# Kernel tuning notes

Measured on AMD Instinct MI355X. Metric: run time of the kernel, lower is better.

The kernel has to match this reference:

```python
import jax, jax.numpy as jnp
import numpy as np

N_NODES = 50000

def sage_conv(x, src, dst, W_l, b_l, W_r):
    # mean-aggregate neighbor features x[src] at dst, then lin_l(agg)+lin_r(x)
    msgs = x[src]                                       # [E, d]
    agg = jax.ops.segment_sum(msgs, dst, num_segments=N_NODES)
    cnt = jax.ops.segment_sum(jnp.ones((src.shape[0],), x.dtype), dst, num_segments=N_NODES)
    agg = agg / jnp.maximum(cnt, 1.0)[:, None]          # [N, d]
    return agg @ W_l.T + b_l + x @ W_r.T


def setup_inputs() -> dict:
    key = jax.random.key(0)
    ks = jax.random.split(key, 10)
    in_c, hid, out_c = 128, 128, 64
    x = jax.random.normal(ks[0], (N_NODES, in_c), dtype=jnp.float32)
    edge_index = jax.random.randint(ks[1], (2, 800000), 0, N_NODES, dtype=jnp.int64)
    s = 1.0 / np.sqrt(in_c)
    W1_l = jax.random.uniform(ks[2], (hid, in_c), minval=-s, maxval=s)
    b1 = jax.random.uniform(ks[3], (hid,), minval=-s, maxval=s)
    W1_r = jax.random.uniform(ks[4], (hid, in_c), minval=-s, maxval=s)
    s = 1.0 / np.sqrt(hid)
    W2_l = jax.random.uniform(ks[5], (hid, hid), minval=-s, maxval=s)
    b2 = jax.random.uniform(ks[6], (hid,), minval=-s, maxval=s)
    W2_r = jax.random.uniform(ks[7], (hid, hid), minval=-s, maxval=s)
    W3 = jax.random.uniform(ks[8], (out_c, hid), minval=-s, maxval=s)
    b3 = jax.random.uniform(ks[9], (out_c,), minval=-s, maxval=s)
    return {"x": x, "edge_index": edge_index, "W1_l": W1_l, "b1": b1, "W1_r": W1_r,
            "W2_l": W2_l, "b2": b2, "W2_r": W2_r, "W3": W3, "b3": b3}


def reference(x, edge_index, W1_l, b1, W1_r, W2_l, b2, W2_r, W3, b3):
    src, dst = edge_index[0], edge_index[1]
    h = jax.nn.relu(sage_conv(x, src, dst, W1_l, b1, W1_r))
    h = jax.nn.relu(sage_conv(h, src, dst, W2_l, b2, W2_r))
    return h @ W3.T + b3
```

## Files before the change

### kernel.cpp

```cpp
#include <hip/hip_runtime.h>

#define FDIM 128

typedef __attribute__((ext_vector_type(8))) short bf16x8;
typedef __attribute__((ext_vector_type(4))) float f32x4;

static __device__ __forceinline__ ushort f2bf(float f) {
    uint u = __float_as_uint(f);
    uint r = (u + 0x7FFF + ((u >> 16) & 1)) >> 16;
    return (ushort)r;
}
static __device__ __forceinline__ uint packbf(float lo, float hi) {
    return (uint)f2bf(lo) | ((uint)f2bf(hi) << 16);
}
static __device__ __forceinline__ float bflo(uint v) { return __uint_as_float(v << 16); }
static __device__ __forceinline__ float bfhi(uint v) { return __uint_as_float(v & 0xFFFF0000u); }


__global__ void prep_kernel(const float* __restrict__ x, ushort* __restrict__ xb, int nx8,
                            const float* __restrict__ W1l, const float* __restrict__ W1r,
                            const float* __restrict__ W2l, const float* __restrict__ W2r,
                            const float* __restrict__ W3, ushort* __restrict__ wbuf,
                            const int* __restrict__ dst, int E, int* __restrict__ bcnt,
                            int nconv) {
    const int b = blockIdx.x;
    const int tid = threadIdx.x;
    if (b < nconv) {
        int i = b * 256 + tid;
        if (i < nx8) {
            const float* s = x + (size_t)i * 8;
            float4 a = *(const float4*)(s);
            float4 c = *(const float4*)(s + 4);
            uint4 o;
            o.x = packbf(a.x, a.y); o.y = packbf(a.z, a.w);
            o.z = packbf(c.x, c.y); o.w = packbf(c.z, c.w);
            *(uint4*)(xb + (size_t)i * 8) = o;
        }
    } else if (b < nconv + 36) {
        int c = (b - nconv) * 256 + tid;
        const float* s; ushort* d;
        if (c < 2048)      { s = W1l + (size_t)c * 8;          d = wbuf + (size_t)c * 8; }
        else if (c < 4096) { s = W1r + (size_t)(c - 2048) * 8; d = wbuf + 16384 + (size_t)(c - 2048) * 8; }
        else if (c < 6144) { s = W2l + (size_t)(c - 4096) * 8; d = wbuf + 32768 + (size_t)(c - 4096) * 8; }
        else if (c < 8192) { s = W2r + (size_t)(c - 6144) * 8; d = wbuf + 49152 + (size_t)(c - 6144) * 8; }
        else               { s = W3  + (size_t)(c - 8192) * 8; d = wbuf + 65536 + (size_t)(c - 8192) * 8; }
        float4 a = *(const float4*)(s);
        float4 cc = *(const float4*)(s + 4);
        uint4 o;
        o.x = packbf(a.x, a.y); o.y = packbf(a.z, a.w);
        o.z = packbf(cc.x, cc.y); o.w = packbf(cc.z, cc.w);
        *(uint4*)d = o;
    } else {
        __shared__ int lh[256];
        int hb = b - nconv - 36;
        lh[tid] = 0;
        __syncthreads();
        #pragma unroll
        for (int k = 0; k < 8; ++k) {
            int e = hb * 2048 + k * 256 + tid;
            if (e < E) atomicAdd(&lh[dst[e] >> 8], 1);
        }
        __syncthreads();
        if (lh[tid]) atomicAdd(&bcnt[tid], lh[tid]);
    }
}


__global__ void scan_buckets(const int* __restrict__ bcnt, int* __restrict__ bbase,
                             int* __restrict__ bcur, int nb) {
    const int lane = threadIdx.x;
    const int i0 = lane * 4;
    int v0 = (i0 + 0 < nb) ? bcnt[i0 + 0] : 0;
    int v1 = (i0 + 1 < nb) ? bcnt[i0 + 1] : 0;
    int v2 = (i0 + 2 < nb) ? bcnt[i0 + 2] : 0;
    int v3 = (i0 + 3 < nb) ? bcnt[i0 + 3] : 0;
    int s = v0 + v1 + v2 + v3;
    int incl = s;
    #pragma unroll
    for (int d = 1; d < 64; d <<= 1) {
        int t = __shfl_up(incl, d);
        if (lane >= d) incl += t;
    }
    int excl = incl - s;
    int e0 = excl, e1 = excl + v0, e2 = e1 + v1, e3 = e2 + v2;
    if (i0 + 0 < nb) { bbase[i0 + 0] = e0; bcur[i0 + 0] = e0; }
    if (i0 + 1 < nb) { bbase[i0 + 1] = e1; bcur[i0 + 1] = e1; }
    if (i0 + 2 < nb) { bbase[i0 + 2] = e2; bcur[i0 + 2] = e2; }
    if (i0 + 3 < nb) { bbase[i0 + 3] = e3; bcur[i0 + 3] = e3; }
    int total = __shfl(incl, 63);
    if (lane == 0) bbase[nb] = total;
}


__global__ void pair_scatter(const int* __restrict__ src, const int* __restrict__ dst,
                             int* __restrict__ bcur, uint2* __restrict__ pairs, int E) {
    __shared__ int lh[256];
    __shared__ int gb[256];
    const int tid = threadIdx.x;
    lh[tid] = 0;
    __syncthreads();
    int ss[8], dd[8], sl[8];
    #pragma unroll
    for (int k = 0; k < 8; ++k) {
        int e = blockIdx.x * 2048 + k * 256 + tid;
        if (e < E) {
            ss[k] = src[e];
            dd[k] = dst[e];
            sl[k] = atomicAdd(&lh[dd[k] >> 8], 1);
        } else dd[k] = -1;
    }
    __syncthreads();
    if (lh[tid]) gb[tid] = atomicAdd(&bcur[tid], lh[tid]);
    __syncthreads();
    #pragma unroll
    for (int k = 0; k < 8; ++k) {
        if (dd[k] >= 0) pairs[gb[dd[k] >> 8] + sl[k]] = make_uint2((uint)ss[k], (uint)dd[k]);
    }
}


__global__ void bucket_csr(const uint2* __restrict__ pairs, const int* __restrict__ bbase,
                           int* __restrict__ off, int* __restrict__ csr, int N) {
    __shared__ int cnt[256];
    __shared__ int base[256];
    __shared__ int cur[256];
    const int b = blockIdx.x;
    const int tid = threadIdx.x;
    const int p0 = bbase[b], p1 = bbase[b + 1];
    cnt[tid] = 0;
    __syncthreads();
    for (int p = p0 + tid; p < p1; p += 256) atomicAdd(&cnt[pairs[p].y & 255], 1);
    __syncthreads();
    if (tid < 64) {
        int i0 = tid * 4;
        int v0 = cnt[i0], v1 = cnt[i0 + 1], v2 = cnt[i0 + 2], v3 = cnt[i0 + 3];
        int s = v0 + v1 + v2 + v3;
        int incl = s;
        #pragma unroll
        for (int d = 1; d < 64; d <<= 1) {
            int t = __shfl_up(incl, d);
            if (tid >= d) incl += t;
        }
        int excl = incl - s;
        base[i0] = excl; base[i0 + 1] = excl + v0;
        base[i0 + 2] = excl + v0 + v1; base[i0 + 3] = excl + v0 + v1 + v2;
        cur[i0] = base[i0]; cur[i0 + 1] = base[i0 + 1];
        cur[i0 + 2] = base[i0 + 2]; cur[i0 + 3] = base[i0 + 3];
    }
    __syncthreads();
    int node = (b << 8) + tid;
    if (node <= N) off[node] = p0 + base[tid];
    for (int p = p0 + tid; p < p1; p += 256) {
        uint2 e = pairs[p];
        int slot = atomicAdd(&cur[e.y & 255], 1);
        csr[p0 + slot] = (int)e.x;
    }
}


__global__ void agg_kernel(const ushort* __restrict__ feat, const int* __restrict__ off,
                           const int* __restrict__ csr, ushort* __restrict__ agg, int n) {
    int node = blockIdx.x * 4 + (threadIdx.x >> 6);
    if (node >= n) return;
    const int lane = threadIdx.x & 63;
    const int g = lane >> 4;
    const int c = lane & 15;
    const int j0 = off[node], j1 = off[node + 1];
    float a[8] = {0.f, 0.f, 0.f, 0.f, 0.f, 0.f, 0.f, 0.f};
    for (int j = j0 + g; j < j1; j += 4) {
        int s = csr[j];
        uint4 v = *(const uint4*)(feat + (size_t)s * FDIM + c * 8);
        a[0] += bflo(v.x); a[1] += bfhi(v.x);
        a[2] += bflo(v.y); a[3] += bfhi(v.y);
        a[4] += bflo(v.z); a[5] += bfhi(v.z);
        a[6] += bflo(v.w); a[7] += bfhi(v.w);
    }
    #pragma unroll
    for (int k = 0; k < 8; ++k) {
        a[k] += __shfl_xor(a[k], 16);
        a[k] += __shfl_xor(a[k], 32);
    }
    if (g == 0) {
        float inv = 1.0f / fmaxf((float)(j1 - j0), 1.0f);
        uint4 o;
        o.x = packbf(a[0] * inv, a[1] * inv);
        o.y = packbf(a[2] * inv, a[3] * inv);
        o.z = packbf(a[4] * inv, a[5] * inv);
        o.w = packbf(a[6] * inv, a[7] * inv);
        *(uint4*)(agg + (size_t)node * FDIM + c * 8) = o;
    }
}


template<int RELU>
__global__ void sage_linear_mfma(const ushort* __restrict__ agg, const ushort* __restrict__ xin,
                                 const ushort* __restrict__ Wl, const ushort* __restrict__ Wr,
                                 const float* __restrict__ bias, ushort* __restrict__ out, int n) {
    __shared__ __align__(16) ushort As[32 * FDIM];
    __shared__ __align__(16) ushort Xs[32 * FDIM];
    const int row0 = blockIdx.x * 32;
    const int lane = threadIdx.x & 63;
    const int wid  = threadIdx.x >> 6;
    const int wrow = wid & 1;
    const int wcol = wid >> 1;

    const float4 z4 = make_float4(0.f, 0.f, 0.f, 0.f);
    #pragma unroll
    for (int i = 0; i < 2; ++i) {
        int s = threadIdx.x + i * 256;
        int r = s >> 4, cch = s & 15;
        int row = row0 + r;
        float4 va = z4, vx = z4;
        if (row < n) {
            va = *(const float4*)(agg + (size_t)row * FDIM + cch * 8);
            vx = *(const float4*)(xin + (size_t)row * FDIM + cch * 8);
        }
        int sc = cch ^ (r & 7);
        *(float4*)(As + (r * 16 + sc) * 8) = va;
        *(float4*)(Xs + (r * 16 + sc) * 8) = vx;
    }
    __syncthreads();

    const int lr = lane & 15;
    const int lk = lane >> 4;

    f32x4 acc[4];
    #pragma unroll
    for (int t = 0; t < 4; ++t) acc[t] = (f32x4){0.f, 0.f, 0.f, 0.f};

    const int arow = wrow * 16 + lr;
    #pragma unroll
    for (int ks = 0; ks < 4; ++ks) {
        bf16x8 a = *(const bf16x8*)(As + (arow * 16 + ((ks * 4 + lk) ^ (arow & 7))) * 8);
        #pragma unroll
        for (int t = 0; t < 4; ++t) {
            int wr = wcol * 64 + t * 16 + lr;
            bf16x8 bb = *(const bf16x8*)(Wl + (size_t)wr * FDIM + ks * 32 + lk * 8);
            acc[t] = __builtin_amdgcn_mfma_f32_16x16x32_bf16(a, bb, acc[t], 0, 0, 0);
        }
    }
    #pragma unroll
    for (int ks = 0; ks < 4; ++ks) {
        bf16x8 a = *(const bf16x8*)(Xs + (arow * 16 + ((ks * 4 + lk) ^ (arow & 7))) * 8);
        #pragma unroll
        for (int t = 0; t < 4; ++t) {
            int wr = wcol * 64 + t * 16 + lr;
            bf16x8 bb = *(const bf16x8*)(Wr + (size_t)wr * FDIM + ks * 32 + lk * 8);
            acc[t] = __builtin_amdgcn_mfma_f32_16x16x32_bf16(a, bb, acc[t], 0, 0, 0);
        }
    }

    #pragma unroll
    for (int t = 0; t < 4; ++t) {
        int col = wcol * 64 + t * 16 + lr;
        float bc = bias[col];
        #pragma unroll
        for (int j = 0; j < 4; ++j) {
            int row = row0 + wrow * 16 + lk * 4 + j;
            if (row < n) {
                float v = acc[t][j] + bc;
                if (RELU) v = fmaxf(v, 0.f);
                out[(size_t)row * FDIM + col] = f2bf(v);
            }
        }
    }
}


__global__ void final_mfma(const ushort* __restrict__ h, const ushort* __restrict__ W3,
                           const float* __restrict__ b3, float* __restrict__ out, int n) {
    __shared__ __align__(16) ushort Hs[32 * FDIM];
    const int row0 = blockIdx.x * 32;
    const int lane = threadIdx.x & 63;
    const int wid  = threadIdx.x >> 6;
    const int wrow = wid & 1;
    const int wcol = wid >> 1;

    const float4 z4 = make_float4(0.f, 0.f, 0.f, 0.f);
    #pragma unroll
    for (int i = 0; i < 2; ++i) {
        int s = threadIdx.x + i * 256;
        int r = s >> 4, cch = s & 15;
        int row = row0 + r;
        float4 vh = (row < n) ? *(const float4*)(h + (size_t)row * FDIM + cch * 8) : z4;
        int sc = cch ^ (r & 7);
        *(float4*)(Hs + (r * 16 + sc) * 8) = vh;
    }
    __syncthreads();

    const int lr = lane & 15;
    const int lk = lane >> 4;

    f32x4 acc[2];
    #pragma unroll
    for (int t = 0; t < 2; ++t) acc[t] = (f32x4){0.f, 0.f, 0.f, 0.f};

    const int arow = wrow * 16 + lr;
    #pragma unroll
    for (int ks = 0; ks < 4; ++ks) {
        bf16x8 a = *(const bf16x8*)(Hs + (arow * 16 + ((ks * 4 + lk) ^ (arow & 7))) * 8);
        #pragma unroll
        for (int t = 0; t < 2; ++t) {
            int wr = wcol * 32 + t * 16 + lr;
            bf16x8 bb = *(const bf16x8*)(W3 + (size_t)wr * FDIM + ks * 32 + lk * 8);
            acc[t] = __builtin_amdgcn_mfma_f32_16x16x32_bf16(a, bb, acc[t], 0, 0, 0);
        }
    }

    #pragma unroll
    for (int t = 0; t < 2; ++t) {
        int col = wcol * 32 + t * 16 + lr;
        float bc = b3[col];
        #pragma unroll
        for (int j = 0; j < 4; ++j) {
            int row = row0 + wrow * 16 + lk * 4 + j;
            if (row < n) out[(size_t)row * 64 + col] = acc[t][j] + bc;
        }
    }
}


extern "C" void kernel_launch(void* const* d_in, const int* in_sizes, int n_in,
                              void* d_out, int out_size, void* d_ws, size_t ws_size,
                              hipStream_t stream) {
    const float* x   = (const float*)d_in[0];
    const int*   ei  = (const int*)d_in[1];
    const float* W1l = (const float*)d_in[2];
    const float* b1  = (const float*)d_in[3];
    const float* W1r = (const float*)d_in[4];
    const float* W2l = (const float*)d_in[5];
    const float* b2  = (const float*)d_in[6];
    const float* W2r = (const float*)d_in[7];
    const float* W3  = (const float*)d_in[8];
    const float* b3  = (const float*)d_in[9];
    float* out = (float*)d_out;

    const int N = in_sizes[0] / FDIM;
    const int E = in_sizes[1] / 2;
    const int* src = ei;
    const int* dst = ei + E;
    const int NBK = (N + 255) >> 8;

    char* ws = (char*)d_ws;
    size_t p = 0;
    auto alloc = [&](size_t bytes) {
        char* q = ws + p;
        p += (bytes + 255) & ~(size_t)255;
        return q;
    };
    int* bcnt    = (int*)alloc(256 * 4);
    int* bbase   = (int*)alloc(260 * 4);
    int* bcur    = (int*)alloc(256 * 4);
    uint2* pairs = (uint2*)alloc((size_t)E * 8);
    int* csr     = (int*)alloc((size_t)E * 4);
    int* off     = (int*)alloc((size_t)(N + 1) * 4);
    ushort* xb   = (ushort*)alloc((size_t)N * FDIM * 2);
    ushort* agb  = (ushort*)alloc((size_t)N * FDIM * 2);
    ushort* h1b  = (ushort*)alloc((size_t)N * FDIM * 2);
    ushort* wbuf = (ushort*)alloc(73728 * 2);
    ushort* w1l = wbuf, *w1r = wbuf + 16384, *w2l = wbuf + 32768,
           *w2r = wbuf + 49152, *w3 = wbuf + 65536;
    ushort* h2b = xb;

    hipMemsetAsync(bcnt, 0, 256 * 4, stream);

    const int nx8   = N * FDIM / 8;
    const int nconv = (nx8 + 255) / 256;
    const int nhist = (E + 2047) / 2048;
    prep_kernel<<<nconv + 36 + nhist, 256, 0, stream>>>(
        x, xb, nx8, W1l, W1r, W2l, W2r, W3, wbuf, dst, E, bcnt, nconv);
    scan_buckets<<<1, 64, 0, stream>>>(bcnt, bbase, bcur, NBK);
    pair_scatter<<<(E + 2047) / 2048, 256, 0, stream>>>(src, dst, bcur, pairs, E);
    bucket_csr<<<NBK, 256, 0, stream>>>(pairs, bbase, off, csr, N);

    const int lgrid = (N + 31) / 32;
    agg_kernel<<<(N + 3) / 4, 256, 0, stream>>>(xb, off, csr, agb, N);
    sage_linear_mfma<1><<<lgrid, 256, 0, stream>>>(agb, xb, w1l, w1r, b1, h1b, N);
    agg_kernel<<<(N + 3) / 4, 256, 0, stream>>>(h1b, off, csr, agb, N);
    sage_linear_mfma<1><<<lgrid, 256, 0, stream>>>(agb, h1b, w2l, w2r, b2, h2b, N);
    final_mfma<<<lgrid, 256, 0, stream>>>(h2b, w3, b3, out, N);
}
```

Baseline: 199.7 us.

## Fuse second SAGE linear with output head, pack edge pairs, unroll gather

The second SAGE linear layer and the final projection now run in one kernel. The ReLU'd hidden tile stays in shared memory as bf16 instead of being written to global memory and read back, and one launch is removed. The edge pairs used for CSR construction are packed into 32 bits (24-bit source index plus the 8-bit local destination), which halves that scratch traffic but assumes node ids fit in 24 bits. The aggregation gather loop is unrolled by four so more independent loads are in flight per lane.

```diff
diff --git a/kernel.cpp b/kernel.cpp
--- a/kernel.cpp
+++ b/kernel.cpp
@@ -93,7 +93,7 @@
 
 
 __global__ void pair_scatter(const int* __restrict__ src, const int* __restrict__ dst,
-                             int* __restrict__ bcur, uint2* __restrict__ pairs, int E) {
+                             int* __restrict__ bcur, uint* __restrict__ pairs, int E) {
     __shared__ int lh[256];
     __shared__ int gb[256];
     const int tid = threadIdx.x;
@@ -114,12 +114,13 @@
     __syncthreads();
     #pragma unroll
     for (int k = 0; k < 8; ++k) {
-        if (dd[k] >= 0) pairs[gb[dd[k] >> 8] + sl[k]] = make_uint2((uint)ss[k], (uint)dd[k]);
-    }
-}
-
-
-__global__ void bucket_csr(const uint2* __restrict__ pairs, const int* __restrict__ bbase,
+        if (dd[k] >= 0)
+            pairs[gb[dd[k] >> 8] + sl[k]] = (uint)ss[k] | ((uint)(dd[k] & 255) << 24);
+    }
+}
+
+
+__global__ void bucket_csr(const uint* __restrict__ pairs, const int* __restrict__ bbase,
                            int* __restrict__ off, int* __restrict__ csr, int N) {
     __shared__ int cnt[256];
     __shared__ int base[256];
@@ -129,7 +130,7 @@
     const int p0 = bbase[b], p1 = bbase[b + 1];
     cnt[tid] = 0;
     __syncthreads();
-    for (int p = p0 + tid; p < p1; p += 256) atomicAdd(&cnt[pairs[p].y & 255], 1);
+    for (int p = p0 + tid; p < p1; p += 256) atomicAdd(&cnt[pairs[p] >> 24], 1);
     __syncthreads();
     if (tid < 64) {
         int i0 = tid * 4;
@@ -151,9 +152,9 @@
     int node = (b << 8) + tid;
     if (node <= N) off[node] = p0 + base[tid];
     for (int p = p0 + tid; p < p1; p += 256) {
-        uint2 e = pairs[p];
-        int slot = atomicAdd(&cur[e.y & 255], 1);
-        csr[p0 + slot] = (int)e.x;
+        uint e = pairs[p];
+        int slot = atomicAdd(&cur[e >> 24], 1);
+        csr[p0 + slot] = (int)(e & 0xFFFFFF);
     }
 }
 
@@ -167,13 +168,38 @@
     const int c = lane & 15;
     const int j0 = off[node], j1 = off[node + 1];
     float a[8] = {0.f, 0.f, 0.f, 0.f, 0.f, 0.f, 0.f, 0.f};
-    for (int j = j0 + g; j < j1; j += 4) {
-        int s = csr[j];
-        uint4 v = *(const uint4*)(feat + (size_t)s * FDIM + c * 8);
-        a[0] += bflo(v.x); a[1] += bfhi(v.x);
-        a[2] += bflo(v.y); a[3] += bfhi(v.y);
-        a[4] += bflo(v.z); a[5] += bfhi(v.z);
-        a[6] += bflo(v.w); a[7] += bfhi(v.w);
+    int j = j0 + g;
+    for (; j + 12 < j1; j += 16) {
+        int s0 = csr[j], s1 = csr[j + 4], s2 = csr[j + 8], s3 = csr[j + 12];
+        uint4 v0 = *(const uint4*)(feat + (size_t)s0 * FDIM + c * 8);
+        uint4 v1 = *(const uint4*)(feat + (size_t)s1 * FDIM + c * 8);
+        uint4 v2 = *(const uint4*)(feat + (size_t)s2 * FDIM + c * 8);
+        uint4 v3 = *(const uint4*)(feat + (size_t)s3 * FDIM + c * 8);
+        a[0] += bflo(v0.x) + bflo(v1.x) + bflo(v2.x) + bflo(v3.x);
+        a[1] += bfhi(v0.x) + bfhi(v1.x) + bfhi(v2.x) + bfhi(v3.x);
+        a[2] += bflo(v0.y) + bflo(v1.y) + bflo(v2.y) + bflo(v3.y);
+        a[3] += bfhi(v0.y) + bfhi(v1.y) + bfhi(v2.y) + bfhi(v3.y);
+        a[4] += bflo(v0.z) + bflo(v1.z) + bflo(v2.z) + bflo(v3.z);
+        a[5] += bfhi(v0.z) + bfhi(v1.z) + bfhi(v2.z) + bfhi(v3.z);
+        a[6] += bflo(v0.w) + bflo(v1.w) + bflo(v2.w) + bflo(v3.w);
+        a[7] += bfhi(v0.w) + bfhi(v1.w) + bfhi(v2.w) + bfhi(v3.w);
+    }
+    for (; j + 4 < j1; j += 8) {
+        int s0 = csr[j], s1 = csr[j + 4];
+        uint4 v0 = *(const uint4*)(feat + (size_t)s0 * FDIM + c * 8);
+        uint4 v1 = *(const uint4*)(feat + (size_t)s1 * FDIM + c * 8);
+        a[0] += bflo(v0.x) + bflo(v1.x); a[1] += bfhi(v0.x) + bfhi(v1.x);
+        a[2] += bflo(v0.y) + bflo(v1.y); a[3] += bfhi(v0.y) + bfhi(v1.y);
+        a[4] += bflo(v0.z) + bflo(v1.z); a[5] += bfhi(v0.z) + bfhi(v1.z);
+        a[6] += bflo(v0.w) + bflo(v1.w); a[7] += bfhi(v0.w) + bfhi(v1.w);
+    }
+    for (; j < j1; j += 4) {
+        int s0 = csr[j];
+        uint4 v0 = *(const uint4*)(feat + (size_t)s0 * FDIM + c * 8);
+        a[0] += bflo(v0.x); a[1] += bfhi(v0.x);
+        a[2] += bflo(v0.y); a[3] += bfhi(v0.y);
+        a[4] += bflo(v0.z); a[5] += bfhi(v0.z);
+        a[6] += bflo(v0.w); a[7] += bfhi(v0.w);
     }
     #pragma unroll
     for (int k = 0; k < 8; ++k) {
@@ -267,9 +293,13 @@
 }
 
 
-__global__ void final_mfma(const ushort* __restrict__ h, const ushort* __restrict__ W3,
-                           const float* __restrict__ b3, float* __restrict__ out, int n) {
-    __shared__ __align__(16) ushort Hs[32 * FDIM];
+__global__ void sage_linear2_head(const ushort* __restrict__ agg, const ushort* __restrict__ xin,
+                                  const ushort* __restrict__ Wl, const ushort* __restrict__ Wr,
+                                  const float* __restrict__ bias,
+                                  const ushort* __restrict__ W3, const float* __restrict__ b3,
+                                  float* __restrict__ out, int n) {
+    __shared__ __align__(16) ushort As[32 * FDIM];
+    __shared__ __align__(16) ushort Xs[32 * FDIM];
     const int row0 = blockIdx.x * 32;
     const int lane = threadIdx.x & 63;
     const int wid  = threadIdx.x >> 6;
@@ -282,28 +312,72 @@
         int s = threadIdx.x + i * 256;
         int r = s >> 4, cch = s & 15;
         int row = row0 + r;
-        float4 vh = (row < n) ? *(const float4*)(h + (size_t)row * FDIM + cch * 8) : z4;
+        float4 va = z4, vx = z4;
+        if (row < n) {
+            va = *(const float4*)(agg + (size_t)row * FDIM + cch * 8);
+            vx = *(const float4*)(xin + (size_t)row * FDIM + cch * 8);
+        }
         int sc = cch ^ (r & 7);
-        *(float4*)(Hs + (r * 16 + sc) * 8) = vh;
+        *(float4*)(As + (r * 16 + sc) * 8) = va;
+        *(float4*)(Xs + (r * 16 + sc) * 8) = vx;
     }
     __syncthreads();
 
     const int lr = lane & 15;
     const int lk = lane >> 4;
 
-    f32x4 acc[2];
-    #pragma unroll
-    for (int t = 0; t < 2; ++t) acc[t] = (f32x4){0.f, 0.f, 0.f, 0.f};
+    f32x4 acc[4];
+    #pragma unroll
+    for (int t = 0; t < 4; ++t) acc[t] = (f32x4){0.f, 0.f, 0.f, 0.f};
 
     const int arow = wrow * 16 + lr;
     #pragma unroll
     for (int ks = 0; ks < 4; ++ks) {
-        bf16x8 a = *(const bf16x8*)(Hs + (arow * 16 + ((ks * 4 + lk) ^ (arow & 7))) * 8);
+        bf16x8 a = *(const bf16x8*)(As + (arow * 16 + ((ks * 4 + lk) ^ (arow & 7))) * 8);
+        #pragma unroll
+        for (int t = 0; t < 4; ++t) {
+            int wr = wcol * 64 + t * 16 + lr;
+            bf16x8 bb = *(const bf16x8*)(Wl + (size_t)wr * FDIM + ks * 32 + lk * 8);
+            acc[t] = __builtin_amdgcn_mfma_f32_16x16x32_bf16(a, bb, acc[t], 0, 0, 0);
+        }
+    }
+    #pragma unroll
+    for (int ks = 0; ks < 4; ++ks) {
+        bf16x8 a = *(const bf16x8*)(Xs + (arow * 16 + ((ks * 4 + lk) ^ (arow & 7))) * 8);
+        #pragma unroll
+        for (int t = 0; t < 4; ++t) {
+            int wr = wcol * 64 + t * 16 + lr;
+            bf16x8 bb = *(const bf16x8*)(Wr + (size_t)wr * FDIM + ks * 32 + lk * 8);
+            acc[t] = __builtin_amdgcn_mfma_f32_16x16x32_bf16(a, bb, acc[t], 0, 0, 0);
+        }
+    }
+
+    __syncthreads();
+    #pragma unroll
+    for (int t = 0; t < 4; ++t) {
+        int col = wcol * 64 + t * 16 + lr;
+        float bc = bias[col];
+        #pragma unroll
+        for (int j = 0; j < 4; ++j) {
+            int r = wrow * 16 + lk * 4 + j;
+            float v = fmaxf(acc[t][j] + bc, 0.f);
+            As[(r * 16 + ((col >> 3) ^ (r & 7))) * 8 + (col & 7)] = f2bf(v);
+        }
+    }
+    __syncthreads();
+
+    f32x4 acc2[2];
+    #pragma unroll
+    for (int t = 0; t < 2; ++t) acc2[t] = (f32x4){0.f, 0.f, 0.f, 0.f};
+
+    #pragma unroll
+    for (int ks = 0; ks < 4; ++ks) {
+        bf16x8 a = *(const bf16x8*)(As + (arow * 16 + ((ks * 4 + lk) ^ (arow & 7))) * 8);
         #pragma unroll
         for (int t = 0; t < 2; ++t) {
             int wr = wcol * 32 + t * 16 + lr;
             bf16x8 bb = *(const bf16x8*)(W3 + (size_t)wr * FDIM + ks * 32 + lk * 8);
-            acc[t] = __builtin_amdgcn_mfma_f32_16x16x32_bf16(a, bb, acc[t], 0, 0, 0);
+            acc2[t] = __builtin_amdgcn_mfma_f32_16x16x32_bf16(a, bb, acc2[t], 0, 0, 0);
         }
     }
 
@@ -314,7 +388,7 @@
         #pragma unroll
         for (int j = 0; j < 4; ++j) {
             int row = row0 + wrow * 16 + lk * 4 + j;
-            if (row < n) out[(size_t)row * 64 + col] = acc[t][j] + bc;
+            if (row < n) out[(size_t)row * 64 + col] = acc2[t][j] + bc;
         }
     }
 }
@@ -351,7 +425,7 @@
     int* bcnt    = (int*)alloc(256 * 4);
     int* bbase   = (int*)alloc(260 * 4);
     int* bcur    = (int*)alloc(256 * 4);
-    uint2* pairs = (uint2*)alloc((size_t)E * 8);
+    uint* pairs  = (uint*)alloc((size_t)E * 4);
     int* csr     = (int*)alloc((size_t)E * 4);
     int* off     = (int*)alloc((size_t)(N + 1) * 4);
     ushort* xb   = (ushort*)alloc((size_t)N * FDIM * 2);
@@ -360,7 +434,6 @@
     ushort* wbuf = (ushort*)alloc(73728 * 2);
     ushort* w1l = wbuf, *w1r = wbuf + 16384, *w2l = wbuf + 32768,
            *w2r = wbuf + 49152, *w3 = wbuf + 65536;
-    ushort* h2b = xb;
 
     hipMemsetAsync(bcnt, 0, 256 * 4, stream);
 
@@ -377,6 +450,5 @@
     agg_kernel<<<(N + 3) / 4, 256, 0, stream>>>(xb, off, csr, agb, N);
     sage_linear_mfma<1><<<lgrid, 256, 0, stream>>>(agb, xb, w1l, w1r, b1, h1b, N);
     agg_kernel<<<(N + 3) / 4, 256, 0, stream>>>(h1b, off, csr, agb, N);
-    sage_linear_mfma<1><<<lgrid, 256, 0, stream>>>(agb, h1b, w2l, w2r, b2, h2b, N);
-    final_mfma<<<lgrid, 256, 0, stream>>>(h2b, w3, b3, out, N);
-}
+    sage_linear2_head<<<lgrid, 256, 0, stream>>>(agb, h1b, w2l, w2r, b2, w3, b3, out, N);
+}
```

Measured after the change: 181.3 us. -9.2%, faster.
